# Performance work log

Measured on AMD Instinct MI355X. Metric: run time of the kernel, lower is better.

## Reference

```python
import jax, jax.numpy as jnp
import numpy as np

MARGIN = 0.3
EPS = 1e-8  # torch CosineSimilarity eps


def setup_inputs() -> dict:
    key = jax.random.key(0)
    k1, k2 = jax.random.split(key)
    x = jax.random.normal(k1, (8192, 1024), dtype=jnp.float32)
    y = jax.random.normal(k2, (8192, 1024), dtype=jnp.float32)
    return {"x": x, "y": y}


def _rank(S):
    # S[i, j] = cos(a_i, b_j); positives on the diagonal.
    d = jnp.diagonal(S)                      # [N] positive similarities
    E = jnp.exp(S)                           # [N, N]
    neg = jnp.sum(E, axis=1) - jnp.exp(d)    # sum over j != i of exp(S[i, j])
    m1 = jnp.exp(d - MARGIN)
    ret = -jnp.log(m1 / (m1 + neg))          # per-anchor AMS loss
    return jnp.mean(ret)


def reference(x, y):
    xn = x / jnp.maximum(jnp.linalg.norm(x, axis=-1, keepdims=True), EPS)
    yn = y / jnp.maximum(jnp.linalg.norm(y, axis=-1, keepdims=True), EPS)
    S = xn @ yn.T                            # [N, N] full cosine-similarity matrix
    # calculate_loss = rank(x, y) + rank(y, x); rank(y, x) uses S.T
    return _rank(S) + _rank(S.T)
```

## Files before the change

### kernel.cpp

```cpp
#include <hip/hip_runtime.h>
#include <hip/hip_bf16.h>
#include <math.h>

#define NROWS 8192
#define DDIM  1024
#define BT    128
#define NBLK  (NROWS / BT)
#define MARGIN 0.3f
#define INV1024 0.0009765625f

typedef __attribute__((ext_vector_type(4))) float  f32x4;
typedef __attribute__((ext_vector_type(8))) __bf16 bf16x8;
typedef __attribute__((ext_vector_type(4))) int    i32x4;
typedef __attribute__((ext_vector_type(8))) int    i32x8;

__device__ __forceinline__ unsigned f2bf_bits(float f) {
  unsigned u = __float_as_uint(f);
  u += 0x7fffu + ((u >> 16) & 1u);
  return u >> 16;
}

__device__ __forceinline__ unsigned q4(float u) {
  float a = fabsf(u);
  unsigned c = (unsigned)(a > 0.25f) + (unsigned)(a > 0.75f) + (unsigned)(a > 1.25f)
             + (unsigned)(a > 1.75f) + (unsigned)(a > 2.5f)  + (unsigned)(a > 3.5f)
             + (unsigned)(a > 5.0f);
  return c | ((__float_as_uint(u) >> 28) & 8u);
}

__global__ __launch_bounds__(256) void normconv4_kernel(const float* __restrict__ x,
                                                        const float* __restrict__ y,
                                                        unsigned short* __restrict__ xq4,
                                                        unsigned short* __restrict__ yq4,
                                                        float* __restrict__ zero_base) {
  if (blockIdx.x < 16) {
    ((float4*)zero_base)[blockIdx.x * 256 + threadIdx.x] = (float4){0.f, 0.f, 0.f, 0.f};
  }
  int wid  = blockIdx.x * 4 + (threadIdx.x >> 6);
  int lane = threadIdx.x & 63;
  bool isx = (wid < NROWS);
  const float* src = isx ? x : y;
  unsigned short* dst = isx ? xq4 : yq4;
  int row = isx ? wid : (wid - NROWS);
  const float4* p = (const float4*)(src + (size_t)row * DDIM);
  float4 v[4];
  float s = 0.f;
#pragma unroll
  for (int a = 0; a < 4; ++a) {
    v[a] = p[a * 64 + lane];
    s = fmaf(v[a].x, v[a].x, s); s = fmaf(v[a].y, v[a].y, s);
    s = fmaf(v[a].z, v[a].z, s); s = fmaf(v[a].w, v[a].w, s);
  }
#pragma unroll
  for (int m = 1; m < 64; m <<= 1) s += __shfl_xor(s, m, 64);
  float inv = 32.0f / fmaxf(sqrtf(s), 1e-8f);
  unsigned short* drow = dst + (size_t)row * 256;
#pragma unroll
  for (int a = 0; a < 4; ++a) {
    unsigned n0 = q4(v[a].x * inv), n1 = q4(v[a].y * inv);
    unsigned n2 = q4(v[a].z * inv), n3 = q4(v[a].w * inv);
    drow[a * 64 + lane] = (unsigned short)(n0 | (n1 << 4) | (n2 << 8) | (n3 << 12));
  }
}

__global__ __launch_bounds__(256, 4) void gemm_mx4_kernel(const unsigned char* __restrict__ xq4,
                                                          const unsigned char* __restrict__ yq4,
                                                          float* __restrict__ rowsum,
                                                          float* __restrict__ colsum,
                                                          float* __restrict__ diagv) {
  __shared__ alignas(16) unsigned char As[2][BT * 64];
  __shared__ alignas(16) unsigned char Bs[2][BT * 64];
  __shared__ float red_row[BT];
  __shared__ float red_col[BT];

  const int tid  = threadIdx.x;
  const int bi   = blockIdx.y;
  const int bj   = blockIdx.x;
  const int lane = tid & 63;
  const int wave = tid >> 6;
  const int wr   = wave >> 1, wc = wave & 1;
  const int quad = lane >> 4, l15 = lane & 15;

  if (tid < BT) red_row[tid] = 0.f; else red_col[tid - BT] = 0.f;

  const int r_l = lane >> 2;
  const int cg  = (lane & 3) ^ ((lane >> 3) & 3);
  const unsigned char* ga = xq4 + (size_t)(bi * BT + wave * 32 + r_l) * 512 + cg * 16;
  const unsigned char* gb = yq4 + (size_t)(bj * BT + wave * 32 + r_l) * 512 + cg * 16;

#define STAGE(buf, kb)                                                          \
  {                                                                             \
    _Pragma("unroll")                                                           \
    for (int a = 0; a < 2; ++a) {                                               \
      __builtin_amdgcn_global_load_lds(                                         \
          (const __attribute__((address_space(1))) unsigned int*)(ga + (size_t)a * 16 * 512 + (kb)), \
          (__attribute__((address_space(3))) unsigned int*)&As[buf][(wave * 32 + a * 16) * 64], \
          16, 0, 0);                                                            \
      __builtin_amdgcn_global_load_lds(                                         \
          (const __attribute__((address_space(1))) unsigned int*)(gb + (size_t)a * 16 * 512 + (kb)), \
          (__attribute__((address_space(3))) unsigned int*)&Bs[buf][(wave * 32 + a * 16) * 64], \
          16, 0, 0);                                                            \
    }                                                                           \
  }

  f32x4 acc[4][4];
#pragma unroll
  for (int i = 0; i < 4; ++i)
#pragma unroll
    for (int j = 0; j < 4; ++j) acc[i][j] = (f32x4){0.f, 0.f, 0.f, 0.f};

  const int pg = (quad ^ ((l15 >> 1) & 3)) * 16;

  STAGE(0, 0);
#pragma unroll
  for (int it = 0; it < 8; ++it) {
    const int cur = it & 1;
    __syncthreads();
    if (it < 7) STAGE(cur ^ 1, (it + 1) * 64);
    i32x4 b4[4];
#pragma unroll
    for (int f = 0; f < 4; ++f)
      b4[f] = *(const i32x4*)&Bs[cur][(wc * 64 + f * 16 + l15) * 64 + pg];
#pragma unroll
    for (int fr = 0; fr < 4; ++fr) {
      i32x4 a4 = *(const i32x4*)&As[cur][(wr * 64 + fr * 16 + l15) * 64 + pg];
      i32x8 af = (i32x8){a4.x, a4.y, a4.z, a4.w, 0, 0, 0, 0};
#pragma unroll
      for (int fc = 0; fc < 4; ++fc) {
        i32x8 bf = (i32x8){b4[fc].x, b4[fc].y, b4[fc].z, b4[fc].w, 0, 0, 0, 0};
        acc[fr][fc] = __builtin_amdgcn_mfma_scale_f32_16x16x128_f8f6f4(
            af, bf, acc[fr][fc],
            4, 4,
            0, 0x7F7F7F7F,
            0, 0x7F7F7F7F);
      }
    }
  }
#undef STAGE

  if (bi == bj && wr == wc && (l15 >> 2) == quad) {
    int r = l15 & 3;
#pragma unroll
    for (int f = 0; f < 4; ++f)
      diagv[bi * BT + wr * 64 + f * 16 + l15] = acc[f][f][r] * INV1024;
  }

  float racc[4][4];
  float cacc[4];
#pragma unroll
  for (int i = 0; i < 4; ++i) {
    cacc[i] = 0.f;
#pragma unroll
    for (int j = 0; j < 4; ++j) racc[i][j] = 0.f;
  }
#pragma unroll
  for (int fr = 0; fr < 4; ++fr)
#pragma unroll
    for (int fc = 0; fc < 4; ++fc) {
      f32x4 v = acc[fr][fc];
#pragma unroll
      for (int r = 0; r < 4; ++r) {
        float e = __expf(v[r] * INV1024);
        racc[fr][r] += e;
        cacc[fc]    += e;
      }
    }
#pragma unroll
  for (int m = 1; m <= 8; m <<= 1)
#pragma unroll
    for (int fr = 0; fr < 4; ++fr)
#pragma unroll
      for (int r = 0; r < 4; ++r) racc[fr][r] += __shfl_xor(racc[fr][r], m, 64);
  if (l15 == 0)
#pragma unroll
    for (int fr = 0; fr < 4; ++fr)
#pragma unroll
      for (int r = 0; r < 4; ++r)
        atomicAdd(&red_row[wr * 64 + fr * 16 + quad * 4 + r], racc[fr][r]);
#pragma unroll
  for (int m = 16; m <= 32; m <<= 1)
#pragma unroll
    for (int fc = 0; fc < 4; ++fc) cacc[fc] += __shfl_xor(cacc[fc], m, 64);
  if (quad == 0)
#pragma unroll
    for (int fc = 0; fc < 4; ++fc)
      atomicAdd(&red_col[wc * 64 + fc * 16 + l15], cacc[fc]);

  __syncthreads();
  if (tid < BT) atomicAdd(&rowsum[bi * BT + tid], red_row[tid]);
  else          atomicAdd(&colsum[bj * BT + (tid - BT)], red_col[tid - BT]);
}

__global__ __launch_bounds__(256) void norm_kernel(const float* __restrict__ x,
                                                   const float* __restrict__ y,
                                                   float* __restrict__ invn) {
  int wid  = (int)((blockIdx.x * blockDim.x + threadIdx.x) >> 6);
  int lane = threadIdx.x & 63;
  const float* src = (wid < NROWS) ? x : y;
  int row = (wid < NROWS) ? wid : (wid - NROWS);
  const float4* p = (const float4*)(src + (size_t)row * DDIM);
  float s = 0.f;
#pragma unroll
  for (int a = 0; a < 4; ++a) {
    float4 v = p[a * 64 + lane];
    s = fmaf(v.x, v.x, s); s = fmaf(v.y, v.y, s);
    s = fmaf(v.z, v.z, s); s = fmaf(v.w, v.w, s);
  }
#pragma unroll
  for (int m = 1; m < 64; m <<= 1) s += __shfl_xor(s, m, 64);
  if (lane == 0) invn[wid] = 1.0f / fmaxf(sqrtf(s), 1e-8f);
}

__global__ __launch_bounds__(256) void gemm_kernel(const float* __restrict__ x,
                                                   const float* __restrict__ y,
                                                   const float* __restrict__ invn,
                                                   float* __restrict__ rowsum,
                                                   float* __restrict__ colsum,
                                                   float* __restrict__ diagv) {
  __shared__ alignas(16) unsigned short As[BT * 64];
  __shared__ alignas(16) unsigned short Bs[BT * 64];
  __shared__ float red_row[BT];
  __shared__ float red_col[BT];

  const int tid  = threadIdx.x;
  const int bi   = blockIdx.y;
  const int bj   = blockIdx.x;
  const int lane = tid & 63;
  const int wave = tid >> 6;
  const int wr   = wave >> 1, wc = wave & 1;
  const int quad = lane >> 4, l15 = lane & 15;
  const int srow = tid >> 4;
  const int sc4  = tid & 15;

  if (tid < BT) red_row[tid] = 0.f; else red_col[tid - BT] = 0.f;

  float ainv[8], binv[8];
#pragma unroll
  for (int a = 0; a < 8; ++a) {
    ainv[a] = invn[bi * BT + a * 16 + srow];
    binv[a] = invn[NROWS + bj * BT + a * 16 + srow];
  }

  f32x4 acc[4][4];
#pragma unroll
  for (int i = 0; i < 4; ++i)
#pragma unroll
    for (int j = 0; j < 4; ++j) acc[i][j] = (f32x4){0.f, 0.f, 0.f, 0.f};

  for (int k0 = 0; k0 < DDIM; k0 += 64) {
#pragma unroll
    for (int a = 0; a < 8; ++a) {
      int row = a * 16 + srow;
      float4 va = *(const float4*)(x + (size_t)(bi * BT + row) * DDIM + k0 + sc4 * 4);
      float4 vb = *(const float4*)(y + (size_t)(bj * BT + row) * DDIM + k0 + sc4 * 4);
      float sa = ainv[a], sb = binv[a];
      unsigned long long pa =
          (unsigned long long)f2bf_bits(va.x * sa) |
          ((unsigned long long)f2bf_bits(va.y * sa) << 16) |
          ((unsigned long long)f2bf_bits(va.z * sa) << 32) |
          ((unsigned long long)f2bf_bits(va.w * sa) << 48);
      unsigned long long pb =
          (unsigned long long)f2bf_bits(vb.x * sb) |
          ((unsigned long long)f2bf_bits(vb.y * sb) << 16) |
          ((unsigned long long)f2bf_bits(vb.z * sb) << 32) |
          ((unsigned long long)f2bf_bits(vb.w * sb) << 48);
      *(unsigned long long*)&As[row * 64 + sc4 * 4] = pa;
      *(unsigned long long*)&Bs[row * 64 + sc4 * 4] = pb;
    }
    __syncthreads();
#pragma unroll
    for (int kk = 0; kk < 64; kk += 32) {
      bf16x8 af[4], bf[4];
#pragma unroll
      for (int f = 0; f < 4; ++f) {
        af[f] = *(const bf16x8*)&As[(wr * 64 + f * 16 + l15) * 64 + kk + quad * 8];
        bf[f] = *(const bf16x8*)&Bs[(wc * 64 + f * 16 + l15) * 64 + kk + quad * 8];
      }
#pragma unroll
      for (int fr = 0; fr < 4; ++fr)
#pragma unroll
        for (int fc = 0; fc < 4; ++fc)
          acc[fr][fc] = __builtin_amdgcn_mfma_f32_16x16x32_bf16(af[fr], bf[fc], acc[fr][fc], 0, 0, 0);
    }
    __syncthreads();
  }

  if (bi == bj && wr == wc && (l15 >> 2) == quad) {
    int r = l15 & 3;
#pragma unroll
    for (int f = 0; f < 4; ++f)
      diagv[bi * BT + wr * 64 + f * 16 + l15] = acc[f][f][r];
  }

  float racc[4][4];
  float cacc[4];
#pragma unroll
  for (int i = 0; i < 4; ++i) {
    cacc[i] = 0.f;
#pragma unroll
    for (int j = 0; j < 4; ++j) racc[i][j] = 0.f;
  }
#pragma unroll
  for (int fr = 0; fr < 4; ++fr)
#pragma unroll
    for (int fc = 0; fc < 4; ++fc) {
      f32x4 v = acc[fr][fc];
#pragma unroll
      for (int r = 0; r < 4; ++r) {
        float e = __expf(v[r]);
        racc[fr][r] += e;
        cacc[fc]    += e;
      }
    }
#pragma unroll
  for (int m = 1; m <= 8; m <<= 1)
#pragma unroll
    for (int fr = 0; fr < 4; ++fr)
#pragma unroll
      for (int r = 0; r < 4; ++r) racc[fr][r] += __shfl_xor(racc[fr][r], m, 64);
  if (l15 == 0)
#pragma unroll
    for (int fr = 0; fr < 4; ++fr)
#pragma unroll
      for (int r = 0; r < 4; ++r)
        atomicAdd(&red_row[wr * 64 + fr * 16 + quad * 4 + r], racc[fr][r]);
#pragma unroll
  for (int m = 16; m <= 32; m <<= 1)
#pragma unroll
    for (int fc = 0; fc < 4; ++fc) cacc[fc] += __shfl_xor(cacc[fc], m, 64);
  if (quad == 0)
#pragma unroll
    for (int fc = 0; fc < 4; ++fc)
      atomicAdd(&red_col[wc * 64 + fc * 16 + l15], cacc[fc]);

  __syncthreads();
  if (tid < BT) atomicAdd(&rowsum[bi * BT + tid], red_row[tid]);
  else          atomicAdd(&colsum[bj * BT + (tid - BT)], red_col[tid - BT]);
}

__global__ __launch_bounds__(1024) void finalize_kernel(const float* __restrict__ rowsum,
                                                        const float* __restrict__ colsum,
                                                        const float* __restrict__ diagv,
                                                        float* __restrict__ out) {
  float s = 0.f;
  for (int i = threadIdx.x; i < NROWS; i += 1024) {
    float d  = diagv[i];
    float ed = __expf(d);
    float m1 = __expf(d - MARGIN);
    float negR = rowsum[i] - ed;
    float negC = colsum[i] - ed;
    s += __logf((m1 + negR) / m1) + __logf((m1 + negC) / m1);
  }
  __shared__ float red[16];
#pragma unroll
  for (int m = 1; m < 64; m <<= 1) s += __shfl_xor(s, m, 64);
  if ((threadIdx.x & 63) == 0) red[threadIdx.x >> 6] = s;
  __syncthreads();
  if (threadIdx.x < 64) {
    float v = (threadIdx.x < 16) ? red[threadIdx.x] : 0.f;
#pragma unroll
    for (int m = 1; m < 16; m <<= 1) v += __shfl_xor(v, m, 64);
    if (threadIdx.x == 0) out[0] = v / (float)NROWS;
  }
}

extern "C" void kernel_launch(void* const* d_in, const int* in_sizes, int n_in,
                              void* d_out, int out_size, void* d_ws, size_t ws_size,
                              hipStream_t stream) {
  const float* x = (const float*)d_in[0];
  const float* y = (const float*)d_in[1];
  float* out = (float*)d_out;
  char* ws = (char*)d_ws;

  const size_t q_bytes = (size_t)NROWS * 512;
  const size_t need_fast = 2 * q_bytes + 3 * NROWS * 4;

  if (ws_size >= need_fast) {
    unsigned short* xq4 = (unsigned short*)ws;
    unsigned short* yq4 = (unsigned short*)(ws + q_bytes);
    float* rowsum = (float*)(ws + 2 * q_bytes);
    float* colsum = rowsum + NROWS;
    float* diagv  = colsum + NROWS;
    normconv4_kernel<<<dim3((2 * NROWS) / 4), 256, 0, stream>>>(x, y, xq4, yq4, rowsum);
    gemm_mx4_kernel<<<dim3(NBLK, NBLK), 256, 0, stream>>>(
        (const unsigned char*)xq4, (const unsigned char*)yq4, rowsum, colsum, diagv);
    finalize_kernel<<<dim3(1), 1024, 0, stream>>>(rowsum, colsum, diagv, out);
  } else {
    float* invn   = (float*)ws;
    float* rowsum = (float*)(ws + 16384 * 4);
    float* colsum = rowsum + NROWS;
    float* diagv  = colsum + NROWS;
    hipMemsetAsync(rowsum, 0, 2 * NROWS * sizeof(float), stream);
    norm_kernel<<<dim3((2 * NROWS) / 4 / 64), 256, 0, stream>>>(x, y, invn);
    gemm_kernel<<<dim3(NROWS / BT, NROWS / BT), 256, 0, stream>>>(x, y, invn, rowsum, colsum, diagv);
    finalize_kernel<<<dim3(1), 1024, 0, stream>>>(rowsum, colsum, diagv, out);
  }
}
```

Baseline: 156.2 us.

## Make MX4 GEMM persistent over four tiles with cross-tile prefetch

The 4096-block 2D grid is replaced by 1024 blocks that each loop over four output tiles. The last k-step of each tile prefetches the first k-slice of the next tile into the LDS buffer, which hides the load latency at tile boundaries and cuts per-block launch and prologue cost. The exp call is also changed to exp2f with a pre-scaled constant (1/1024 times log2 e), saving one multiply. The cost is a longer-lived block, extra shared-memory reset work per tile, and a different tile order that may change L2 reuse.

```diff
diff --git a/kernel.cpp b/kernel.cpp
--- a/kernel.cpp
+++ b/kernel.cpp
@@ -8,6 +8,7 @@
 #define NBLK  (NROWS / BT)
 #define MARGIN 0.3f
 #define INV1024 0.0009765625f
+#define EXPSC   0.0014088551f
 
 typedef __attribute__((ext_vector_type(4))) float  f32x4;
 typedef __attribute__((ext_vector_type(8))) __bf16 bf16x8;
@@ -74,121 +75,131 @@
   __shared__ float red_col[BT];
 
   const int tid  = threadIdx.x;
-  const int bi   = blockIdx.y;
-  const int bj   = blockIdx.x;
   const int lane = tid & 63;
   const int wave = tid >> 6;
   const int wr   = wave >> 1, wc = wave & 1;
   const int quad = lane >> 4, l15 = lane & 15;
 
-  if (tid < BT) red_row[tid] = 0.f; else red_col[tid - BT] = 0.f;
-
-  const int r_l = lane >> 2;
-  const int cg  = (lane & 3) ^ ((lane >> 3) & 3);
-  const unsigned char* ga = xq4 + (size_t)(bi * BT + wave * 32 + r_l) * 512 + cg * 16;
-  const unsigned char* gb = yq4 + (size_t)(bj * BT + wave * 32 + r_l) * 512 + cg * 16;
-
-#define STAGE(buf, kb)                                                          \
+  const unsigned lbase = (unsigned)(wave * 16384 + (lane >> 2) * 512
+                                    + (((lane & 3) ^ ((lane >> 3) & 3)) << 4));
+  const int pg = (quad ^ ((l15 >> 1) & 3)) * 16;
+
+#define STAGE(buf, gA, gB, kb)                                                  \
   {                                                                             \
     _Pragma("unroll")                                                           \
     for (int a = 0; a < 2; ++a) {                                               \
       __builtin_amdgcn_global_load_lds(                                         \
-          (const __attribute__((address_space(1))) unsigned int*)(ga + (size_t)a * 16 * 512 + (kb)), \
+          (const __attribute__((address_space(1))) unsigned int*)((gA) + lbase + a * 8192 + (kb)), \
           (__attribute__((address_space(3))) unsigned int*)&As[buf][(wave * 32 + a * 16) * 64], \
           16, 0, 0);                                                            \
       __builtin_amdgcn_global_load_lds(                                         \
-          (const __attribute__((address_space(1))) unsigned int*)(gb + (size_t)a * 16 * 512 + (kb)), \
+          (const __attribute__((address_space(1))) unsigned int*)((gB) + lbase + a * 8192 + (kb)), \
           (__attribute__((address_space(3))) unsigned int*)&Bs[buf][(wave * 32 + a * 16) * 64], \
           16, 0, 0);                                                            \
     }                                                                           \
   }
 
-  f32x4 acc[4][4];
-#pragma unroll
-  for (int i = 0; i < 4; ++i)
-#pragma unroll
-    for (int j = 0; j < 4; ++j) acc[i][j] = (f32x4){0.f, 0.f, 0.f, 0.f};
-
-  const int pg = (quad ^ ((l15 >> 1) & 3)) * 16;
-
-  STAGE(0, 0);
-#pragma unroll
-  for (int it = 0; it < 8; ++it) {
-    const int cur = it & 1;
+  const int t0 = blockIdx.x;
+  int bi = t0 >> 6, bj = t0 & 63;
+  const unsigned char* gA = xq4 + ((size_t)bi << 16);
+  const unsigned char* gB = yq4 + ((size_t)bj << 16);
+
+  if (tid < BT) red_row[tid] = 0.f; else red_col[tid - BT] = 0.f;
+  STAGE(0, gA, gB, 0);
+
+  for (int ti = 0; ti < 4; ++ti) {
+    const int tn  = t0 + (ti + 1) * 1024;
+    const int bin = (tn >> 6) & 63, bjn = tn & 63;
+    const unsigned char* gAn = xq4 + ((size_t)bin << 16);
+    const unsigned char* gBn = yq4 + ((size_t)bjn << 16);
+
+    f32x4 acc[4][4];
+#pragma unroll
+    for (int i = 0; i < 4; ++i)
+#pragma unroll
+      for (int j = 0; j < 4; ++j) acc[i][j] = (f32x4){0.f, 0.f, 0.f, 0.f};
+
+#pragma unroll
+    for (int it = 0; it < 8; ++it) {
+      const int cur = it & 1;
+      __syncthreads();
+      if (it < 7)      STAGE(cur ^ 1, gA, gB, (it + 1) * 64)
+      else if (ti < 3) STAGE(0, gAn, gBn, 0)
+      i32x8 bf[4];
+#pragma unroll
+      for (int f = 0; f < 4; ++f) {
+        i32x4 b4 = *(const i32x4*)&Bs[cur][(wc * 64 + f * 16 + l15) * 64 + pg];
+        bf[f] = (i32x8){b4.x, b4.y, b4.z, b4.w, 0, 0, 0, 0};
+      }
+#pragma unroll
+      for (int fr = 0; fr < 4; ++fr) {
+        i32x4 a4 = *(const i32x4*)&As[cur][(wr * 64 + fr * 16 + l15) * 64 + pg];
+        i32x8 af = (i32x8){a4.x, a4.y, a4.z, a4.w, 0, 0, 0, 0};
+#pragma unroll
+        for (int fc = 0; fc < 4; ++fc)
+          acc[fr][fc] = __builtin_amdgcn_mfma_scale_f32_16x16x128_f8f6f4(
+              af, bf[fc], acc[fr][fc],
+              4, 4,
+              0, 0x7F7F7F7F,
+              0, 0x7F7F7F7F);
+      }
+    }
+
+    if (bi == bj && wr == wc && (l15 >> 2) == quad) {
+      int r = l15 & 3;
+#pragma unroll
+      for (int f = 0; f < 4; ++f)
+        diagv[bi * BT + wr * 64 + f * 16 + l15] = acc[f][f][r] * INV1024;
+    }
+
+    float racc[4][4];
+    float cacc[4];
+#pragma unroll
+    for (int i = 0; i < 4; ++i) {
+      cacc[i] = 0.f;
+#pragma unroll
+      for (int j = 0; j < 4; ++j) racc[i][j] = 0.f;
+    }
+#pragma unroll
+    for (int fr = 0; fr < 4; ++fr)
+#pragma unroll
+      for (int fc = 0; fc < 4; ++fc) {
+        f32x4 v = acc[fr][fc];
+#pragma unroll
+        for (int r = 0; r < 4; ++r) {
+          float e = exp2f(v[r] * EXPSC);
+          racc[fr][r] += e;
+          cacc[fc]    += e;
+        }
+      }
+#pragma unroll
+    for (int m = 1; m <= 8; m <<= 1)
+#pragma unroll
+      for (int fr = 0; fr < 4; ++fr)
+#pragma unroll
+        for (int r = 0; r < 4; ++r) racc[fr][r] += __shfl_xor(racc[fr][r], m, 64);
+    if (l15 == 0)
+#pragma unroll
+      for (int fr = 0; fr < 4; ++fr)
+#pragma unroll
+        for (int r = 0; r < 4; ++r)
+          atomicAdd(&red_row[wr * 64 + fr * 16 + quad * 4 + r], racc[fr][r]);
+#pragma unroll
+    for (int m = 16; m <= 32; m <<= 1)
+#pragma unroll
+      for (int fc = 0; fc < 4; ++fc) cacc[fc] += __shfl_xor(cacc[fc], m, 64);
+    if (quad == 0)
+#pragma unroll
+      for (int fc = 0; fc < 4; ++fc)
+        atomicAdd(&red_col[wc * 64 + fc * 16 + l15], cacc[fc]);
+
     __syncthreads();
-    if (it < 7) STAGE(cur ^ 1, (it + 1) * 64);
-    i32x4 b4[4];
-#pragma unroll
-    for (int f = 0; f < 4; ++f)
-      b4[f] = *(const i32x4*)&Bs[cur][(wc * 64 + f * 16 + l15) * 64 + pg];
-#pragma unroll
-    for (int fr = 0; fr < 4; ++fr) {
-      i32x4 a4 = *(const i32x4*)&As[cur][(wr * 64 + fr * 16 + l15) * 64 + pg];
-      i32x8 af = (i32x8){a4.x, a4.y, a4.z, a4.w, 0, 0, 0, 0};
-#pragma unroll
-      for (int fc = 0; fc < 4; ++fc) {
-        i32x8 bf = (i32x8){b4[fc].x, b4[fc].y, b4[fc].z, b4[fc].w, 0, 0, 0, 0};
-        acc[fr][fc] = __builtin_amdgcn_mfma_scale_f32_16x16x128_f8f6f4(
-            af, bf, acc[fr][fc],
-            4, 4,
-            0, 0x7F7F7F7F,
-            0, 0x7F7F7F7F);
-      }
-    }
+    if (tid < BT) { atomicAdd(&rowsum[bi * BT + tid], red_row[tid]); red_row[tid] = 0.f; }
+    else          { atomicAdd(&colsum[bj * BT + (tid - BT)], red_col[tid - BT]); red_col[tid - BT] = 0.f; }
+
+    gA = gAn; gB = gBn; bi = bin; bj = bjn;
   }
 #undef STAGE
-
-  if (bi == bj && wr == wc && (l15 >> 2) == quad) {
-    int r = l15 & 3;
-#pragma unroll
-    for (int f = 0; f < 4; ++f)
-      diagv[bi * BT + wr * 64 + f * 16 + l15] = acc[f][f][r] * INV1024;
-  }
-
-  float racc[4][4];
-  float cacc[4];
-#pragma unroll
-  for (int i = 0; i < 4; ++i) {
-    cacc[i] = 0.f;
-#pragma unroll
-    for (int j = 0; j < 4; ++j) racc[i][j] = 0.f;
-  }
-#pragma unroll
-  for (int fr = 0; fr < 4; ++fr)
-#pragma unroll
-    for (int fc = 0; fc < 4; ++fc) {
-      f32x4 v = acc[fr][fc];
-#pragma unroll
-      for (int r = 0; r < 4; ++r) {
-        float e = __expf(v[r] * INV1024);
-        racc[fr][r] += e;
-        cacc[fc]    += e;
-      }
-    }
-#pragma unroll
-  for (int m = 1; m <= 8; m <<= 1)
-#pragma unroll
-    for (int fr = 0; fr < 4; ++fr)
-#pragma unroll
-      for (int r = 0; r < 4; ++r) racc[fr][r] += __shfl_xor(racc[fr][r], m, 64);
-  if (l15 == 0)
-#pragma unroll
-    for (int fr = 0; fr < 4; ++fr)
-#pragma unroll
-      for (int r = 0; r < 4; ++r)
-        atomicAdd(&red_row[wr * 64 + fr * 16 + quad * 4 + r], racc[fr][r]);
-#pragma unroll
-  for (int m = 16; m <= 32; m <<= 1)
-#pragma unroll
-    for (int fc = 0; fc < 4; ++fc) cacc[fc] += __shfl_xor(cacc[fc], m, 64);
-  if (quad == 0)
-#pragma unroll
-    for (int fc = 0; fc < 4; ++fc)
-      atomicAdd(&red_col[wc * 64 + fc * 16 + l15], cacc[fc]);
-
-  __syncthreads();
-  if (tid < BT) atomicAdd(&rowsum[bi * BT + tid], red_row[tid]);
-  else          atomicAdd(&colsum[bj * BT + (tid - BT)], red_col[tid - BT]);
 }
 
 __global__ __launch_bounds__(256) void norm_kernel(const float* __restrict__ x,
@@ -382,7 +393,7 @@
     float* colsum = rowsum + NROWS;
     float* diagv  = colsum + NROWS;
     normconv4_kernel<<<dim3((2 * NROWS) / 4), 256, 0, stream>>>(x, y, xq4, yq4, rowsum);
-    gemm_mx4_kernel<<<dim3(NBLK, NBLK), 256, 0, stream>>>(
+    gemm_mx4_kernel<<<dim3(1024), 256, 0, stream>>>(
         (const unsigned char*)xq4, (const unsigned char*)yq4, rowsum, colsum, diagv);
     finalize_kernel<<<dim3(1), 1024, 0, stream>>>(rowsum, colsum, diagv, out);
   } else {
```

After: 595.8 us. +281.5%, slower.
